# Optimization experiments

Measured on AMD Instinct MI355X. Metric: run time of the kernel, lower is better.

The kernel has to match this reference:

```python
import jax, jax.numpy as jnp
import numpy as np


def _normalized_adj(A):
    # get_a: d = 0.5*I, a = off-diagonal ones + A, a2 = d @ a @ d
    off = jnp.array([[0., 1., 1.], [1., 0., 1.], [1., 1., 0.]], dtype=A.dtype)
    a = off + A
    d = 0.5 * jnp.eye(3, dtype=A.dtype)
    return d @ a @ d  # [3,3]


def setup_inputs() -> dict:
    key = jax.random.key(0)
    k1, k2 = jax.random.split(key)
    B = 8192
    x = jax.random.normal(k1, (B, 3, 10), dtype=jnp.float32)
    A = jnp.eye(3, dtype=jnp.float32)  # get_A() returns identity; Parameter init
    stdv = 1.0 / np.sqrt(10.0)
    W = jax.random.uniform(k2, (10, 10), dtype=jnp.float32, minval=-stdv, maxval=stdv)
    return {"x": x, "A": A, "W": W}


def reference(x, A, W):
    # adjacency is detached in the torch forward
    adj = jax.lax.stop_gradient(_normalized_adj(A))  # [3,3], shared across batch
    # GraphConvolution: adj @ (x @ W)
    support = jnp.einsum('bnf,fo->bno', x, W)          # [B,3,10]
    h = jnp.einsum('nm,bmo->bno', adj, support)        # [B,3,10]
    # permute -> [B,10,3]; AvgPool1d(2) on length 3 -> length 1: mean of nodes 0,1
    pooled = 0.5 * (h[:, 0, :] + h[:, 1, :])           # [B,10]
    # ScaleDotProductAttention over the batch axis
    score = jax.nn.softmax(pooled @ pooled.T, axis=-1)  # [B,B]
    v = score @ pooled                                  # [B,10]
    return v
```

## Files before the change

### kernel.cpp

```cpp
#include <hip/hip_runtime.h>
#include <math.h>

#define BROWS 8192
#define F 10
#define NT 16
#define NW 16
#define IB 32
#define SQRT_LOG2E 1.2011224087864498f

#if __has_builtin(__builtin_amdgcn_exp2f)
#define EXP2F(x) __builtin_amdgcn_exp2f(x)
#else
#define EXP2F(x) exp2f(x)
#endif

#define WAITVM(n) __builtin_amdgcn_s_waitcnt(0xF00 | 0x70 | (n))

typedef _Float16 half4 __attribute__((ext_vector_type(4)));
typedef __fp16 fp16x2 __attribute__((ext_vector_type(2)));
typedef float floatx4 __attribute__((ext_vector_type(4)));

__device__ __forceinline__ half4 exp4_to_h4(float a, float b, float c, float d) {
#if __has_builtin(__builtin_amdgcn_cvt_pkrtz)
    union { fp16x2 h2[2]; half4 h4; } u;
    u.h2[0] = __builtin_amdgcn_cvt_pkrtz(EXP2F(a), EXP2F(b));
    u.h2[1] = __builtin_amdgcn_cvt_pkrtz(EXP2F(c), EXP2F(d));
    return u.h4;
#else
    half4 r;
    r[0] = (_Float16)EXP2F(a); r[1] = (_Float16)EXP2F(b);
    r[2] = (_Float16)EXP2F(c); r[3] = (_Float16)EXP2F(d);
    return r;
#endif
}

__device__ __forceinline__ uint32_t pack2(_Float16 a, _Float16 b) {
    union { _Float16 h[2]; uint32_t u; } x;
    x.h[0] = a; x.h[1] = b;
    return x.u;
}

__device__ __forceinline__ void gload_lds16(const void* g, void* l) {
#if __has_builtin(__builtin_amdgcn_global_load_lds)
    __builtin_amdgcn_global_load_lds(
        (const __attribute__((address_space(1))) void*)g,
        (__attribute__((address_space(3))) void*)l, 16, 0, 0);
#else
    *(float4*)l = *(const float4*)g;
#endif
}

__global__ void pooled_kernel(const float* __restrict__ x,
                              const float* __restrict__ A,
                              const float* __restrict__ W,
                              _Float16* __restrict__ q_tiled,
                              _Float16* __restrict__ a_tiled) {
    int b = blockIdx.x * blockDim.x + threadIdx.x;
    if (b >= BROWS) return;

    float c0 = 0.125f * (1.0f + A[0] + A[3]);
    float c1 = 0.125f * (1.0f + A[1] + A[4]);
    float c2 = 0.125f * (2.0f + A[2] + A[5]);

    const float2* xb = (const float2*)(x + (size_t)b * 3 * F);
    float xv[3 * F];
#pragma unroll
    for (int k = 0; k < 15; ++k) {
        float2 t = xb[k];
        xv[2 * k] = t.x; xv[2 * k + 1] = t.y;
    }

    float y[F];
#pragma unroll
    for (int f = 0; f < F; ++f)
        y[f] = c0 * xv[f] + c1 * xv[F + f] + c2 * xv[2 * F + f];

    float po[F];
#pragma unroll
    for (int o = 0; o < F; ++o) {
        float acc = 0.0f;
#pragma unroll
        for (int f = 0; f < F; ++f)
            acc = fmaf(y[f], W[f * F + o], acc);
        po[o] = acc;
    }

    float s = SQRT_LOG2E;
    uint2* qd = (uint2*)(q_tiled + (size_t)b * 16);
    qd[0] = make_uint2(pack2((_Float16)(s*po[0]), (_Float16)(s*po[1])),
                       pack2((_Float16)(s*po[2]), (_Float16)(s*po[3])));
    qd[1] = make_uint2(pack2((_Float16)(s*po[4]), (_Float16)(s*po[5])),
                       pack2((_Float16)(s*po[6]), (_Float16)(s*po[7])));
    qd[2] = make_uint2(pack2((_Float16)(s*po[8]), (_Float16)(s*po[9])), 0u);
    qd[3] = make_uint2(0u, 0u);

    _Float16* at = a_tiled + (size_t)(b >> 5) * 512 + (b & 31);
#pragma unroll
    for (int o = 0; o < F; ++o)
        at[o * 32] = (_Float16)po[o];
    at[10 * 32] = (_Float16)1.0f;
#pragma unroll
    for (int o = 11; o < 16; ++o)
        at[o * 32] = (_Float16)0.0f;
}

__global__ void attn_kernel(const _Float16* __restrict__ q_tiled,
                            const _Float16* __restrict__ a_tiled,
                            float* __restrict__ out) {
    __shared__ __align__(16) _Float16 ring[4][NW][1024];
    float* red = (float*)&ring[0][0][0];

    const int tid  = threadIdx.x;
    const int wave = tid >> 6;
    const int lane = tid & 63;
    const int m    = lane & 15;
    const int quad = lane >> 4;
    const int i0   = blockIdx.x * IB;

    half4 b1a = *(const half4*)(q_tiled + (size_t)(i0 + m) * 16 + quad * 4);
    half4 b1b = *(const half4*)(q_tiled + (size_t)(i0 + 16 + m) * 16 + quad * 4);

    const char* qsrc = (const char*)q_tiled + (size_t)wave * 1024 + lane * 16;
    const char* asrc = (const char*)a_tiled + (size_t)wave * 1024 + lane * 16;

    char* slotp[4];
#pragma unroll
    for (int s = 0; s < 4; ++s)
        slotp[s] = (char*)&ring[s][wave][0] + lane * 16;

#pragma unroll
    for (int s = 0; s < 3; ++s) {
        gload_lds16(qsrc, slotp[s]);
        gload_lds16(asrc, slotp[s] + 1024);
        qsrc += 16 * 1024; asrc += 16 * 1024;
    }

    floatx4 accA0 = {0.f,0.f,0.f,0.f}, accA1 = {0.f,0.f,0.f,0.f};
    floatx4 accB0 = {0.f,0.f,0.f,0.f}, accB1 = {0.f,0.f,0.f,0.f};

    for (int t = 0; t < NT; ++t) {
        if (t < NT - 2)      WAITVM(4);
        else if (t == NT-2)  WAITVM(2);
        else                 WAITVM(0);

        const _Float16* qs  = &ring[t & 3][wave][0];
        const _Float16* as_ = qs + 512;
        half4 a1_0 = *(const half4*)&qs[(0 * 16 + m) * 16 + quad * 4];
        half4 a1_1 = *(const half4*)&qs[(1 * 16 + m) * 16 + quad * 4];
        half4 ag_0 = *(const half4*)&as_[m * 32 + 0 * 16 + quad * 4];
        half4 ag_1 = *(const half4*)&as_[m * 32 + 1 * 16 + quad * 4];

        if (t + 3 < NT) {
            gload_lds16(qsrc, slotp[(t + 3) & 3]);
            gload_lds16(asrc, slotp[(t + 3) & 3] + 1024);
            qsrc += 16 * 1024; asrc += 16 * 1024;
        }

        floatx4 z = {0.f,0.f,0.f,0.f};
        floatx4 d1a0 = __builtin_amdgcn_mfma_f32_16x16x16f16(a1_0, b1a, z, 0, 0, 0);
        floatx4 d1b0 = __builtin_amdgcn_mfma_f32_16x16x16f16(a1_0, b1b, z, 0, 0, 0);
        floatx4 d1a1 = __builtin_amdgcn_mfma_f32_16x16x16f16(a1_1, b1a, z, 0, 0, 0);
        floatx4 d1b1 = __builtin_amdgcn_mfma_f32_16x16x16f16(a1_1, b1b, z, 0, 0, 0);
        half4 a2a0 = exp4_to_h4(d1a0[0], d1a0[1], d1a0[2], d1a0[3]);
        half4 a2b0 = exp4_to_h4(d1b0[0], d1b0[1], d1b0[2], d1b0[3]);
        half4 a2a1 = exp4_to_h4(d1a1[0], d1a1[1], d1a1[2], d1a1[3]);
        half4 a2b1 = exp4_to_h4(d1b1[0], d1b1[1], d1b1[2], d1b1[3]);
        accA0 = __builtin_amdgcn_mfma_f32_16x16x16f16(ag_0, a2a0, accA0, 0, 0, 0);
        accB0 = __builtin_amdgcn_mfma_f32_16x16x16f16(ag_0, a2b0, accB0, 0, 0, 0);
        accA1 = __builtin_amdgcn_mfma_f32_16x16x16f16(ag_1, a2a1, accA1, 0, 0, 0);
        accB1 = __builtin_amdgcn_mfma_f32_16x16x16f16(ag_1, a2b1, accB1, 0, 0, 0);
    }

    floatx4 accA = accA0 + accA1;
    floatx4 accB = accB0 + accB1;

    __syncthreads();
    if (quad < 3) {
        *(floatx4*)&red[((size_t)wave * IB + m) * 12 + quad * 4] = accA;
        *(floatx4*)&red[((size_t)wave * IB + 16 + m) * 12 + quad * 4] = accB;
    }
    __syncthreads();

    if (tid < IB * F) {
        const int i = tid / F;
        const int f = tid % F;
        float sum = 0.0f, l = 0.0f;
#pragma unroll
        for (int w = 0; w < NW; ++w) {
            sum += red[((size_t)w * IB + i) * 12 + f];
            l   += red[((size_t)w * IB + i) * 12 + 10];
        }
        out[(size_t)(i0 + i) * F + f] = sum / l;
    }
}

extern "C" void kernel_launch(void* const* d_in, const int* in_sizes, int n_in,
                              void* d_out, int out_size, void* d_ws, size_t ws_size,
                              hipStream_t stream) {
    const float* x = (const float*)d_in[0];
    const float* A = (const float*)d_in[1];
    const float* W = (const float*)d_in[2];
    float* out = (float*)d_out;

    _Float16* q_tiled = (_Float16*)d_ws;
    _Float16* a_tiled = (_Float16*)((char*)d_ws + 262144);

    pooled_kernel<<<BROWS / 64, 64, 0, stream>>>(x, A, W, q_tiled, a_tiled);
    attn_kernel<<<BROWS / IB, NW * 64, 0, stream>>>(q_tiled, a_tiled, out);
}
```

Before: 69.80 us.

## Parallelize pooled kernel across output features and fully unroll attention loop

The pooled kernel now stages 16 rows of x in shared memory and gives each thread one (row, output feature) pair, instead of one thread computing a whole row. This uses 512 blocks of 256 threads instead of 128 blocks of 64, so many more lanes are active and the global loads are coalesced. The attention loop is fully unrolled, and the ring-slot pointers are computed inline rather than kept in a register array. The trade-off is extra shared-memory traffic, a barrier, and scattered 2-byte stores.

```diff
diff --git a/kernel.cpp b/kernel.cpp
--- a/kernel.cpp
+++ b/kernel.cpp
@@ -6,6 +6,7 @@
 #define NT 16
 #define NW 16
 #define IB 32
+#define PB 16
 #define SQRT_LOG2E 1.2011224087864498f
 
 #if __has_builtin(__builtin_amdgcn_exp2f)
@@ -34,12 +35,6 @@
 #endif
 }
 
-__device__ __forceinline__ uint32_t pack2(_Float16 a, _Float16 b) {
-    union { _Float16 h[2]; uint32_t u; } x;
-    x.h[0] = a; x.h[1] = b;
-    return x.u;
-}
-
 __device__ __forceinline__ void gload_lds16(const void* g, void* l) {
 #if __has_builtin(__builtin_amdgcn_global_load_lds)
     __builtin_amdgcn_global_load_lds(
@@ -55,53 +50,41 @@
                               const float* __restrict__ W,
                               _Float16* __restrict__ q_tiled,
                               _Float16* __restrict__ a_tiled) {
-    int b = blockIdx.x * blockDim.x + threadIdx.x;
-    if (b >= BROWS) return;
+    __shared__ float xs[PB * 30];
+    const int tid = threadIdx.x;
+    const int b0 = blockIdx.x * PB;
 
-    float c0 = 0.125f * (1.0f + A[0] + A[3]);
-    float c1 = 0.125f * (1.0f + A[1] + A[4]);
-    float c2 = 0.125f * (2.0f + A[2] + A[5]);
+    if (tid < 240) {
+        float2 t = ((const float2*)(x + (size_t)b0 * 30))[tid];
+        xs[2 * tid] = t.x;
+        xs[2 * tid + 1] = t.y;
+    }
+    __syncthreads();
 
-    const float2* xb = (const float2*)(x + (size_t)b * 3 * F);
-    float xv[3 * F];
+    const int r = tid >> 4;
+    const int o = tid & 15;
+    const int b = b0 + r;
+
+    const float c0 = 0.125f * (1.0f + A[0] + A[3]);
+    const float c1 = 0.125f * (1.0f + A[1] + A[4]);
+    const float c2 = 0.125f * (2.0f + A[2] + A[5]);
+
+    float po = 0.0f;
+    if (o < F) {
+        const float* xr = &xs[r * 30];
 #pragma unroll
-    for (int k = 0; k < 15; ++k) {
-        float2 t = xb[k];
-        xv[2 * k] = t.x; xv[2 * k + 1] = t.y;
+        for (int f = 0; f < F; ++f) {
+            float y = c0 * xr[f] + c1 * xr[F + f] + c2 * xr[2 * F + f];
+            po = fmaf(y, W[f * F + o], po);
+        }
     }
 
-    float y[F];
-#pragma unroll
-    for (int f = 0; f < F; ++f)
-        y[f] = c0 * xv[f] + c1 * xv[F + f] + c2 * xv[2 * F + f];
+    q_tiled[(size_t)b * 16 + o] =
+        (o < F) ? (_Float16)(SQRT_LOG2E * po) : (_Float16)0.0f;
 
-    float po[F];
-#pragma unroll
-    for (int o = 0; o < F; ++o) {
-        float acc = 0.0f;
-#pragma unroll
-        for (int f = 0; f < F; ++f)
-            acc = fmaf(y[f], W[f * F + o], acc);
-        po[o] = acc;
-    }
-
-    float s = SQRT_LOG2E;
-    uint2* qd = (uint2*)(q_tiled + (size_t)b * 16);
-    qd[0] = make_uint2(pack2((_Float16)(s*po[0]), (_Float16)(s*po[1])),
-                       pack2((_Float16)(s*po[2]), (_Float16)(s*po[3])));
-    qd[1] = make_uint2(pack2((_Float16)(s*po[4]), (_Float16)(s*po[5])),
-                       pack2((_Float16)(s*po[6]), (_Float16)(s*po[7])));
-    qd[2] = make_uint2(pack2((_Float16)(s*po[8]), (_Float16)(s*po[9])), 0u);
-    qd[3] = make_uint2(0u, 0u);
-
-    _Float16* at = a_tiled + (size_t)(b >> 5) * 512 + (b & 31);
-#pragma unroll
-    for (int o = 0; o < F; ++o)
-        at[o * 32] = (_Float16)po[o];
-    at[10 * 32] = (_Float16)1.0f;
-#pragma unroll
-    for (int o = 11; o < 16; ++o)
-        at[o * 32] = (_Float16)0.0f;
+    _Float16 av = (o < F) ? (_Float16)po
+                          : (o == F ? (_Float16)1.0f : (_Float16)0.0f);
+    a_tiled[(size_t)(b >> 5) * 512 + o * 32 + (b & 31)] = av;
 }
 
 __global__ void attn_kernel(const _Float16* __restrict__ q_tiled,
@@ -116,28 +99,26 @@
     const int m    = lane & 15;
     const int quad = lane >> 4;
     const int i0   = blockIdx.x * IB;
+    const int lofs = lane * 16;
 
     half4 b1a = *(const half4*)(q_tiled + (size_t)(i0 + m) * 16 + quad * 4);
     half4 b1b = *(const half4*)(q_tiled + (size_t)(i0 + 16 + m) * 16 + quad * 4);
 
-    const char* qsrc = (const char*)q_tiled + (size_t)wave * 1024 + lane * 16;
-    const char* asrc = (const char*)a_tiled + (size_t)wave * 1024 + lane * 16;
-
-    char* slotp[4];
-#pragma unroll
-    for (int s = 0; s < 4; ++s)
-        slotp[s] = (char*)&ring[s][wave][0] + lane * 16;
+    const char* qsrc = (const char*)q_tiled + (size_t)wave * 1024 + lofs;
+    const char* asrc = (const char*)a_tiled + (size_t)wave * 1024 + lofs;
 
 #pragma unroll
     for (int s = 0; s < 3; ++s) {
-        gload_lds16(qsrc, slotp[s]);
-        gload_lds16(asrc, slotp[s] + 1024);
+        char* dst = (char*)&ring[s][wave][0] + lofs;
+        gload_lds16(qsrc, dst);
+        gload_lds16(asrc, dst + 1024);
         qsrc += 16 * 1024; asrc += 16 * 1024;
     }
 
     floatx4 accA0 = {0.f,0.f,0.f,0.f}, accA1 = {0.f,0.f,0.f,0.f};
     floatx4 accB0 = {0.f,0.f,0.f,0.f}, accB1 = {0.f,0.f,0.f,0.f};
 
+#pragma unroll
     for (int t = 0; t < NT; ++t) {
         if (t < NT - 2)      WAITVM(4);
         else if (t == NT-2)  WAITVM(2);
@@ -151,8 +132,9 @@
         half4 ag_1 = *(const half4*)&as_[m * 32 + 1 * 16 + quad * 4];
 
         if (t + 3 < NT) {
-            gload_lds16(qsrc, slotp[(t + 3) & 3]);
-            gload_lds16(asrc, slotp[(t + 3) & 3] + 1024);
+            char* dst = (char*)&ring[(t + 3) & 3][wave][0] + lofs;
+            gload_lds16(qsrc, dst);
+            gload_lds16(asrc, dst + 1024);
             qsrc += 16 * 1024; asrc += 16 * 1024;
         }
 
@@ -205,6 +187,6 @@
     _Float16* q_tiled = (_Float16*)d_ws;
     _Float16* a_tiled = (_Float16*)((char*)d_ws + 262144);
 
-    pooled_kernel<<<BROWS / 64, 64, 0, stream>>>(x, A, W, q_tiled, a_tiled);
+    pooled_kernel<<<BROWS / PB, 256, 0, stream>>>(x, A, W, q_tiled, a_tiled);
     attn_kernel<<<BROWS / IB, NW * 64, 0, stream>>>(q_tiled, a_tiled, out);
 }
```

Result: faster. 68.36 us (-2.1%).
